# Kernel optimization log

Hardware: AMD Instinct MI355X
Metric: run time of the kernel (lower is better)

Reference implementation:

```python
import jax, jax.numpy as jnp
import numpy as np

GROUP_SIZE = 64  # int4 precision
QMAX = 7.0       # symmetric int4 quant scale divisor


def setup_inputs() -> dict:
    key = jax.random.key(0)
    ks = jax.random.split(key, 8)
    B, S, C_in, C_out, R = 1, 4096, 3072, 3072, 32
    G = C_in // GROUP_SIZE
    x = jax.random.normal(ks[0], (B, S, C_in), dtype=jnp.float32)
    # unpacked int4 weight codes in [0,16); reference subtracts 8 -> signed int4 [-8,7]
    qweight = jax.random.randint(ks[1], (C_out, C_in), 0, 16, dtype=jnp.int32)
    # small positive per-group, per-out-channel weight scales
    wscales = jax.random.uniform(ks[2], (G, C_out), dtype=jnp.float32) * 0.01 + 0.001
    # positive smoothing factors bounded away from zero
    smooth_factor = jax.random.uniform(ks[3], (C_in,), dtype=jnp.float32) + 0.5
    proj_down = jax.random.normal(ks[4], (C_in, R), dtype=jnp.float32) * (1.0 / np.sqrt(C_in))
    proj_up = jax.random.normal(ks[5], (C_out, R), dtype=jnp.float32) * (1.0 / np.sqrt(R))
    bias = jax.random.normal(ks[6], (C_out,), dtype=jnp.float32) * 0.02
    return {
        "x": x,
        "qweight": qweight,
        "wscales": wscales,
        "smooth_factor": smooth_factor,
        "proj_down": proj_down,
        "proj_up": proj_up,
        "bias": bias,
    }


def reference(x, qweight, wscales, smooth_factor, proj_down, proj_up, bias):
    B, S, C = x.shape
    C_out = qweight.shape[0]
    M = B * S
    G = C // GROUP_SIZE

    # --- smoothing: x_hat = x / s (SVDQuant smoothing on activations) ---
    xs = x.reshape(M, C) / smooth_factor  # (M, C)

    # --- low-rank branch hidden state (fused with quantization in CUDA kernel) ---
    lora_act = jnp.einsum('mc,cr->mr', xs, proj_down)  # (M, R)

    # --- dynamic per-token, per-group int4 activation quantization ---
    xg = xs.reshape(M, G, GROUP_SIZE)
    amax = jnp.max(jnp.abs(xg), axis=-1, keepdims=True)          # (M, G, 1)
    ascale = amax / QMAX
    q = jnp.clip(jnp.round(xg / jnp.maximum(ascale, 1e-8)), -8.0, 7.0)
    x_dq = (q * ascale).reshape(M, C)                            # dequantized activations

    # --- weight dequantization: signed int4 codes * per-group/out-channel scales ---
    qw = qweight.astype(jnp.float32) - 8.0                       # (C_out, C) in [-8, 7]
    w_dq = (qw.reshape(C_out, G, GROUP_SIZE) * wscales.T[:, :, None]).reshape(C_out, C)

    # --- quantized GEMM + low-rank correction + bias ---
    out = jnp.einsum('mc,oc->mo', x_dq, w_dq)
    out = out + jnp.einsum('mr,or->mo', lora_act, proj_up) + bias
    return out.reshape(B, S, C_out)
```

## Files before the change

kernel.cpp:

```cpp
#include <hip/hip_runtime.h>
#include <stdint.h>

typedef unsigned short u16;

#define MTOK 4096
#define CIN  3072
#define COUT 3072
#define RANK 32
#define RS   3136
#define LKSPLIT 16
#define LKC (CIN/LKSPLIT)
#define WROWS 6

typedef __attribute__((ext_vector_type(8))) short bf16x8;
typedef __attribute__((ext_vector_type(4))) float f32x4;

__device__ __forceinline__ u16 f2bf(float f) {
  union { float f; unsigned u; } v; v.f = f;
  unsigned r = v.u + 0x7FFFu + ((v.u >> 16) & 1u);
  return (u16)(r >> 16);
}

__device__ __forceinline__ void gload_lds16(const void* g, void* l) {
  __builtin_amdgcn_global_load_lds(
      (const __attribute__((address_space(1))) unsigned int*)g,
      (__attribute__((address_space(3))) unsigned int*)l, 16, 0, 0);
}

__device__ __forceinline__ float quant1(float xs, float ascale, float qd) {
  float q = rintf(xs / qd);
  q = fminf(fmaxf(q, -8.f), 7.f);
  return q * ascale;
}

__global__ __launch_bounds__(256) void prep_kernel(
    const float* __restrict__ x, const float* __restrict__ smooth,
    const int* __restrict__ qw, const float* __restrict__ wsc,
    const float* __restrict__ pd, const float* __restrict__ pu,
    u16* __restrict__ xdq, u16* __restrict__ wdq, u16* __restrict__ pu_bf,
    float* __restrict__ lp)
{
  const int b = blockIdx.x;
  const int t = threadIdx.x;

#pragma unroll
  for (int r = 0; r < WROWS; ++r) {
    const int o = b * WROWS + r;
    const int4* qrow = (const int4*)(qw + (size_t)o * CIN);
    u16* orow = wdq + (size_t)o * RS;
#pragma unroll
    for (int p = 0; p < 3; ++p) {
      const int c4 = p * 256 + t;
      const int g = (c4 * 4) >> 6;
      const float ws = wsc[g * COUT + o];
      const int4 qv = qrow[c4];
      ushort4 ov;
      ov.x = f2bf((float)(qv.x - 8) * ws);
      ov.y = f2bf((float)(qv.y - 8) * ws);
      ov.z = f2bf((float)(qv.z - 8) * ws);
      ov.w = f2bf((float)(qv.w - 8) * ws);
      ((ushort4*)orow)[c4] = ov;
    }
  }
  if (t < WROWS * RANK) {
    const int o = b * WROWS + (t >> 5);
    pu_bf[(size_t)o * RANK + (t & 31)] = f2bf(pu[(size_t)o * RANK + (t & 31)]);
  }

  __shared__ __align__(16) u16 sA[128 * 64];
  __shared__ __align__(16) u16 sB[32 * 64];
  const int m0 = (b >> 4) * 128;
  const int kblk = b & 15;
  const int wave = t >> 6, lane = t & 63;
  const int lm = lane & 15, lkq = (lane >> 4) * 8;

  f32x4 acc[2][2];
  const f32x4 fz = {0.f, 0.f, 0.f, 0.f};
#pragma unroll
  for (int i = 0; i < 2; ++i)
#pragma unroll
    for (int j = 0; j < 2; ++j) acc[i][j] = fz;

  for (int kt = 0; kt < LKC / 64; ++kt) {
    const int k0 = kblk * LKC + kt * 64;
    const int col = (t & 15) * 4;
#pragma unroll
    for (int it = 0; it < 8; ++it) {
      const int row = it * 16 + (t >> 4);
      const float4 xv = *(const float4*)(x + (size_t)(m0 + row) * CIN + k0 + col);
      const float4 sv = *(const float4*)(smooth + k0 + col);
      const float xs0 = xv.x / sv.x, xs1 = xv.y / sv.y;
      const float xs2 = xv.z / sv.z, xs3 = xv.w / sv.w;
      ushort4 ov;
      ov.x = f2bf(xs0); ov.y = f2bf(xs1); ov.z = f2bf(xs2); ov.w = f2bf(xs3);
      *(ushort4*)&sA[row * 64 + col] = ov;
      float a = fmaxf(fmaxf(fabsf(xs0), fabsf(xs1)), fmaxf(fabsf(xs2), fabsf(xs3)));
#pragma unroll
      for (int off = 1; off < 16; off <<= 1) a = fmaxf(a, __shfl_xor(a, off));
      const float ascale = a / 7.0f;
      const float qd = fmaxf(ascale, 1e-8f);
      ushort4 oq;
      oq.x = f2bf(quant1(xs0, ascale, qd));
      oq.y = f2bf(quant1(xs1, ascale, qd));
      oq.z = f2bf(quant1(xs2, ascale, qd));
      oq.w = f2bf(quant1(xs3, ascale, qd));
      *(ushort4*)(xdq + (size_t)(m0 + row) * RS + k0 + col) = oq;
    }
#pragma unroll
    for (int i = 0; i < 8; ++i) {
      const int idx = i * 256 + t;
      const int k = idx >> 5, r = idx & 31;
      sB[r * 64 + k] = f2bf(pd[(size_t)(k0 + k) * RANK + r]);
    }
    __syncthreads();
#pragma unroll
    for (int kk = 0; kk < 2; ++kk) {
      const int ko = kk * 32 + lkq;
      bf16x8 af[2], bfr[2];
#pragma unroll
      for (int i = 0; i < 2; ++i)
        af[i] = *(const bf16x8*)&sA[(wave * 32 + i * 16 + lm) * 64 + ko];
#pragma unroll
      for (int j = 0; j < 2; ++j)
        bfr[j] = *(const bf16x8*)&sB[(j * 16 + lm) * 64 + ko];
#pragma unroll
      for (int i = 0; i < 2; ++i)
#pragma unroll
        for (int j = 0; j < 2; ++j)
          acc[i][j] = __builtin_amdgcn_mfma_f32_16x16x32_bf16(af[i], bfr[j], acc[i][j], 0, 0, 0);
    }
    __syncthreads();
  }
  float* lpk = lp + (size_t)kblk * MTOK * RANK;
#pragma unroll
  for (int i = 0; i < 2; ++i)
#pragma unroll
    for (int j = 0; j < 2; ++j) {
      const int col = j * 16 + lm;
      const int row0 = m0 + wave * 32 + i * 16 + (lane >> 4) * 4;
#pragma unroll
      for (int r = 0; r < 4; ++r)
        lpk[(size_t)(row0 + r) * RANK + col] = acc[i][j][r];
    }
}

__global__ __launch_bounds__(256) void lora_fix_kernel(
    const float* __restrict__ lp, u16* __restrict__ lora_bf)
{
  const int idx = blockIdx.x * 256 + threadIdx.x;
  const int m = idx >> 5, c = idx & 31;
  float s = 0.f;
#pragma unroll
  for (int k = 0; k < LKSPLIT; ++k) s += lp[((size_t)k * MTOK + m) * RANK + c];
  lora_bf[(size_t)m * RANK + c] = f2bf(s);
}


__device__ __forceinline__ void stage_A_half(const u16* __restrict__ g, u16* lds0,
                                             int kt, int half, int buf, int t) {
#pragma unroll
  for (int r = 0; r < 2; ++r) {
    const int id = r * 512 + t;
    const int row = id >> 3;
    const int sl = id & 7;
    const int c16 = sl ^ (row & 7);
    gload_lds16(g + (size_t)(half * 128 + row) * RS + kt * 64 + c16 * 8,
                lds0 + buf * 16384 + half * 8192 + id * 8);
  }
}

__device__ __forceinline__ void stage_B_half(const u16* __restrict__ g, u16* lds0,
                                             int kt, int nh, int buf, int t) {
  u16* base = lds0 + 32768 + buf * 12288 + nh * 6144;
  {
    const int row = t >> 3, sl = t & 7;
    const int c16 = sl ^ (row & 7);
    gload_lds16(g + (size_t)(nh * 96 + row) * RS + kt * 64 + c16 * 8, base + t * 8);
  }
  if (nh ? (t >= 256) : (t < 256)) {
    const int et = t - (nh ? 256 : 0);
    const int row = 64 + (et >> 3), sl = et & 7;
    const int c16 = sl ^ (row & 7);
    gload_lds16(g + (size_t)(nh * 96 + row) * RS + kt * 64 + c16 * 8,
                base + 4096 + et * 8);
  }
}

#define DSA(buf, mh) \
  _Pragma("unroll") for (int i_ = 0; i_ < 2; ++i_) { \
    const int rl = wm * 32 + i_ * 16 + lm; \
    _Pragma("unroll") for (int kk = 0; kk < 2; ++kk) \
      af[i_][kk] = *(const bf16x8*)&lds[(buf)*16384 + (mh)*8192 + rl * 64 + \
                    ((((kk << 2) | q4) ^ (rl & 7)) << 3)]; \
  }

#define DSB(buf, nh, BQ) \
  _Pragma("unroll") for (int j_ = 0; j_ < 3; ++j_) { \
    const int rb = wn * 48 + j_ * 16 + lm; \
    _Pragma("unroll") for (int kk = 0; kk < 2; ++kk) \
      BQ[j_][kk] = *(const bf16x8*)&lds[32768 + (buf)*12288 + (nh)*6144 + rb * 64 + \
                    ((((kk << 2) | q4) ^ (rb & 7)) << 3)]; \
  }

#define MFMA_Q(mh, nh, BQ) \
  __builtin_amdgcn_s_setprio(1); \
  _Pragma("unroll") for (int i_ = 0; i_ < 2; ++i_) \
  _Pragma("unroll") for (int j_ = 0; j_ < 3; ++j_) \
  _Pragma("unroll") for (int kk = 0; kk < 2; ++kk) \
    acc[(mh)*2 + i_][(nh)*3 + j_] = __builtin_amdgcn_mfma_f32_16x16x32_bf16( \
        af[i_][kk], BQ[j_][kk], acc[(mh)*2 + i_][(nh)*3 + j_], 0, 0, 0); \
  __builtin_amdgcn_s_setprio(0);

#define PH_OPEN() \
  __builtin_amdgcn_sched_barrier(0); \
  __builtin_amdgcn_s_barrier(); \
  asm volatile("s_waitcnt lgkmcnt(0)" ::: "memory"); \
  __builtin_amdgcn_sched_barrier(0)

#define PH_CLOSE() \
  __builtin_amdgcn_sched_barrier(0); \
  __builtin_amdgcn_s_barrier(); \
  __builtin_amdgcn_sched_barrier(0)

#define VM7() asm volatile("s_waitcnt vmcnt(7)" ::: "memory")
#define VM0() asm volatile("s_waitcnt vmcnt(0)" ::: "memory")

#define TILE4(cur, S_A0, S_B0, S_B1, S_A1, VMI) do { \
  DSA(cur, 0); DSB(cur, 0, bq0); \
  PH_OPEN(); MFMA_Q(0, 0, bq0); PH_CLOSE(); \
  DSB(cur, 1, bq1); S_A0; S_B0; \
  PH_OPEN(); MFMA_Q(0, 1, bq1); PH_CLOSE(); \
  DSA(cur, 1); S_B1; \
  PH_OPEN(); MFMA_Q(1, 1, bq1); PH_CLOSE(); \
  S_A1; \
  PH_OPEN(); MFMA_Q(1, 0, bq0); VMI; PH_CLOSE(); \
} while (0)

__global__ __launch_bounds__(512, 2) void gemm_kernel(
    const u16* __restrict__ xdq, const u16* __restrict__ wdq,
    const u16* __restrict__ pu_bf, const u16* __restrict__ lora_bf,
    const float* __restrict__ bias, float* __restrict__ out)
{
  __shared__ __align__(16) u16 lds[57344];

  const int t = threadIdx.x;
  const int wid = t >> 6, lane = t & 63;
  const int wm = wid >> 1, wn = wid & 1;
  const int lm = lane & 15, q4 = lane >> 4;

  const int wg = blockIdx.x;
  const int swz = (wg & 7) * 32 + (wg >> 3);
  const int by = swz >> 4, bx = swz & 15;
  const int m0 = by * 256, n0 = bx * 192;

  const u16* Ag = xdq + (size_t)m0 * RS;
  const u16* Bg = wdq + (size_t)n0 * RS;

  f32x4 acc[4][6];
  const f32x4 fz = {0.f, 0.f, 0.f, 0.f};
#pragma unroll
  for (int i = 0; i < 4; ++i)
#pragma unroll
    for (int j = 0; j < 6; ++j) acc[i][j] = fz;

  bf16x8 af[2][2], bq0[3][2], bq1[3][2];

  stage_A_half(Ag, lds, 0, 0, 0, t);
  stage_B_half(Bg, lds, 0, 0, 0, t);
  stage_B_half(Bg, lds, 0, 1, 0, t);
  stage_A_half(Ag, lds, 0, 1, 0, t);
  stage_A_half(Ag, lds, 1, 0, 1, t);
  stage_B_half(Bg, lds, 1, 0, 1, t);
  stage_B_half(Bg, lds, 1, 1, 1, t);
  stage_A_half(Ag, lds, 1, 1, 1, t);
  VM7();
  __builtin_amdgcn_s_barrier();
  __builtin_amdgcn_sched_barrier(0);

  for (int T = 0; T < 46; T += 2) {
    TILE4(0,
          stage_A_half(Ag, lds, T + 2, 0, 0, t),
          stage_B_half(Bg, lds, T + 2, 0, 0, t),
          stage_B_half(Bg, lds, T + 2, 1, 0, t),
          stage_A_half(Ag, lds, T + 2, 1, 0, t),
          VM7());
    TILE4(1,
          stage_A_half(Ag, lds, T + 3, 0, 1, t),
          stage_B_half(Bg, lds, T + 3, 0, 1, t),
          stage_B_half(Bg, lds, T + 3, 1, 1, t),
          stage_A_half(Ag, lds, T + 3, 1, 1, t),
          VM7());
  }
  TILE4(0, (void)0, (void)0, (void)0, (void)0, VM0());
  TILE4(1, (void)0, (void)0, (void)0, (void)0, (void)0);

  bf16x8 bl[6];
#pragma unroll
  for (int b = 0; b < 6; ++b) {
    const int bcol = n0 + (b / 3) * 96 + wn * 48 + (b % 3) * 16 + lm;
    bl[b] = *(const bf16x8*)(pu_bf + (size_t)bcol * RANK + q4 * 8);
  }
#pragma unroll
  for (int a = 0; a < 4; ++a) {
    const int arow = m0 + (a >> 1) * 128 + wm * 32 + (a & 1) * 16 + lm;
    const bf16x8 al = *(const bf16x8*)(lora_bf + (size_t)arow * RANK + q4 * 8);
#pragma unroll
    for (int b = 0; b < 6; ++b)
      acc[a][b] = __builtin_amdgcn_mfma_f32_16x16x32_bf16(al, bl[b], acc[a][b], 0, 0, 0);
  }

#pragma unroll
  for (int b = 0; b < 6; ++b) {
    const int col = n0 + (b / 3) * 96 + wn * 48 + (b % 3) * 16 + lm;
    const float bv = bias[col];
#pragma unroll
    for (int a = 0; a < 4; ++a) {
      const int row0 = m0 + (a >> 1) * 128 + wm * 32 + (a & 1) * 16 + q4 * 4;
#pragma unroll
      for (int r = 0; r < 4; ++r)
        out[(size_t)(row0 + r) * COUT + col] = acc[a][b][r] + bv;
    }
  }
}

extern "C" void kernel_launch(void* const* d_in, const int* in_sizes, int n_in,
                              void* d_out, int out_size, void* d_ws, size_t ws_size,
                              hipStream_t stream) {
  const float* x      = (const float*)d_in[0];
  const int*   qw     = (const int*)d_in[1];
  const float* wsc    = (const float*)d_in[2];
  const float* smooth = (const float*)d_in[3];
  const float* pd     = (const float*)d_in[4];
  const float* pu     = (const float*)d_in[5];
  const float* bias   = (const float*)d_in[6];
  float* out = (float*)d_out;

  u16* xdq     = (u16*)d_ws;
  u16* wdq     = xdq + (size_t)MTOK * RS;
  u16* pu_bf   = wdq + (size_t)COUT * RS;
  u16* lora_bf = pu_bf + (size_t)COUT * RANK;
  float* lp    = (float*)(lora_bf + (size_t)MTOK * RANK);

  prep_kernel<<<512, 256, 0, stream>>>(
      x, smooth, qw, wsc, pd, pu, xdq, wdq, pu_bf, lp);
  lora_fix_kernel<<<MTOK * RANK / 256, 256, 0, stream>>>(lp, lora_bf);
  gemm_kernel<<<256, 512, 0, stream>>>(
      xdq, wdq, pu_bf, lora_bf, bias, out);
}
```

Baseline: 218.3 us.

## Switch GEMM main loop to triple-buffered K=32 tiles with one barrier per tile

The bf16 GEMM main loop moves from double-buffered K=64 tiles, split into four quadrant phases with two barriers each, to triple-buffered K=32 tiles. Each tile now does one stage, one full fragment read and 24 MFMAs, with a single barrier. The LDS swizzle and the vmcnt accounting are reworked to match. The goal is fewer barriers and deeper prefetch to hide global latency, at the cost of less work per barrier and halved K depth per tile, which may leave MFMA bursts too short to cover LDS reads.

```diff
diff --git a/kernel.cpp b/kernel.cpp
--- a/kernel.cpp
+++ b/kernel.cpp
@@ -156,84 +156,70 @@
 }
 
 
-__device__ __forceinline__ void stage_A_half(const u16* __restrict__ g, u16* lds0,
-                                             int kt, int half, int buf, int t) {
+__device__ __forceinline__ void stage32(const u16* __restrict__ Ag,
+                                        const u16* __restrict__ Bg,
+                                        u16* lds, int kt, int buf,
+                                        int t, int wid) {
 #pragma unroll
   for (int r = 0; r < 2; ++r) {
     const int id = r * 512 + t;
-    const int row = id >> 3;
-    const int sl = id & 7;
-    const int c16 = sl ^ (row & 7);
-    gload_lds16(g + (size_t)(half * 128 + row) * RS + kt * 64 + c16 * 8,
-                lds0 + buf * 16384 + half * 8192 + id * 8);
-  }
-}
-
-__device__ __forceinline__ void stage_B_half(const u16* __restrict__ g, u16* lds0,
-                                             int kt, int nh, int buf, int t) {
-  u16* base = lds0 + 32768 + buf * 12288 + nh * 6144;
+    const int row = id >> 2, sl = id & 3;
+    const int c16 = sl ^ ((row >> 1) & 3);
+    gload_lds16(Ag + (size_t)row * RS + kt * 32 + c16 * 8,
+                lds + buf * 8192 + id * 8);
+  }
   {
-    const int row = t >> 3, sl = t & 7;
-    const int c16 = sl ^ (row & 7);
-    gload_lds16(g + (size_t)(nh * 96 + row) * RS + kt * 64 + c16 * 8, base + t * 8);
-  }
-  if (nh ? (t >= 256) : (t < 256)) {
-    const int et = t - (nh ? 256 : 0);
-    const int row = 64 + (et >> 3), sl = et & 7;
-    const int c16 = sl ^ (row & 7);
-    gload_lds16(g + (size_t)(nh * 96 + row) * RS + kt * 64 + c16 * 8,
-                base + 4096 + et * 8);
-  }
-}
-
-#define DSA(buf, mh) \
-  _Pragma("unroll") for (int i_ = 0; i_ < 2; ++i_) { \
-    const int rl = wm * 32 + i_ * 16 + lm; \
-    _Pragma("unroll") for (int kk = 0; kk < 2; ++kk) \
-      af[i_][kk] = *(const bf16x8*)&lds[(buf)*16384 + (mh)*8192 + rl * 64 + \
-                    ((((kk << 2) | q4) ^ (rl & 7)) << 3)]; \
-  }
-
-#define DSB(buf, nh, BQ) \
-  _Pragma("unroll") for (int j_ = 0; j_ < 3; ++j_) { \
-    const int rb = wn * 48 + j_ * 16 + lm; \
-    _Pragma("unroll") for (int kk = 0; kk < 2; ++kk) \
-      BQ[j_][kk] = *(const bf16x8*)&lds[32768 + (buf)*12288 + (nh)*6144 + rb * 64 + \
-                    ((((kk << 2) | q4) ^ (rb & 7)) << 3)]; \
-  }
-
-#define MFMA_Q(mh, nh, BQ) \
+    const int row = t >> 2, sl = t & 3;
+    const int c16 = sl ^ ((row >> 1) & 3);
+    gload_lds16(Bg + (size_t)row * RS + kt * 32 + c16 * 8,
+                lds + 24576 + buf * 6144 + t * 8);
+  }
+  if (wid >= 4) {
+    const int c = 256 + t;
+    const int row = c >> 2, sl = c & 3;
+    const int c16 = sl ^ ((row >> 1) & 3);
+    gload_lds16(Bg + (size_t)row * RS + kt * 32 + c16 * 8,
+                lds + 24576 + buf * 6144 + c * 8);
+  }
+}
+
+#define RD_ALL(BUF) \
+  _Pragma("unroll") for (int a_ = 0; a_ < 4; ++a_) { \
+    const int rl = (a_ >> 1) * 128 + wm * 32 + (a_ & 1) * 16 + lm; \
+    aF[a_] = *(const bf16x8*)&lds[(BUF) * 8192 + rl * 32 + \
+                                  ((q4 ^ ((rl >> 1) & 3)) << 3)]; \
+  } \
+  _Pragma("unroll") for (int b_ = 0; b_ < 6; ++b_) { \
+    const int rb = (b_ / 3) * 96 + wn * 48 + (b_ % 3) * 16 + lm; \
+    bF[b_] = *(const bf16x8*)&lds[24576 + (BUF) * 6144 + rb * 32 + \
+                                  ((q4 ^ ((rb >> 1) & 3)) << 3)]; \
+  }
+
+#define MFMA_ALL() \
   __builtin_amdgcn_s_setprio(1); \
-  _Pragma("unroll") for (int i_ = 0; i_ < 2; ++i_) \
-  _Pragma("unroll") for (int j_ = 0; j_ < 3; ++j_) \
-  _Pragma("unroll") for (int kk = 0; kk < 2; ++kk) \
-    acc[(mh)*2 + i_][(nh)*3 + j_] = __builtin_amdgcn_mfma_f32_16x16x32_bf16( \
-        af[i_][kk], BQ[j_][kk], acc[(mh)*2 + i_][(nh)*3 + j_], 0, 0, 0); \
+  _Pragma("unroll") for (int a_ = 0; a_ < 4; ++a_) \
+  _Pragma("unroll") for (int b_ = 0; b_ < 6; ++b_) \
+    acc[a_][b_] = __builtin_amdgcn_mfma_f32_16x16x32_bf16( \
+        aF[a_], bF[b_], acc[a_][b_], 0, 0, 0); \
   __builtin_amdgcn_s_setprio(0);
 
-#define PH_OPEN() \
-  __builtin_amdgcn_sched_barrier(0); \
-  __builtin_amdgcn_s_barrier(); \
-  asm volatile("s_waitcnt lgkmcnt(0)" ::: "memory"); \
-  __builtin_amdgcn_sched_barrier(0)
-
-#define PH_CLOSE() \
-  __builtin_amdgcn_sched_barrier(0); \
-  __builtin_amdgcn_s_barrier(); \
-  __builtin_amdgcn_sched_barrier(0)
-
-#define VM7() asm volatile("s_waitcnt vmcnt(7)" ::: "memory")
+#define VMB() do { \
+  if (wid < 4) asm volatile("s_waitcnt vmcnt(3)" ::: "memory"); \
+  else         asm volatile("s_waitcnt vmcnt(4)" ::: "memory"); \
+} while (0)
 #define VM0() asm volatile("s_waitcnt vmcnt(0)" ::: "memory")
-
-#define TILE4(cur, S_A0, S_B0, S_B1, S_A1, VMI) do { \
-  DSA(cur, 0); DSB(cur, 0, bq0); \
-  PH_OPEN(); MFMA_Q(0, 0, bq0); PH_CLOSE(); \
-  DSB(cur, 1, bq1); S_A0; S_B0; \
-  PH_OPEN(); MFMA_Q(0, 1, bq1); PH_CLOSE(); \
-  DSA(cur, 1); S_B1; \
-  PH_OPEN(); MFMA_Q(1, 1, bq1); PH_CLOSE(); \
-  S_A1; \
-  PH_OPEN(); MFMA_Q(1, 0, bq0); VMI; PH_CLOSE(); \
+#define LK0() asm volatile("s_waitcnt lgkmcnt(0)" ::: "memory")
+
+#define TILE3(CB, SB, KT2, DOSTAGE, VMW, DOBAR) do { \
+  if (DOSTAGE) stage32(Ag, Bg, lds, (KT2), (SB), t, wid); \
+  RD_ALL(CB); \
+  MFMA_ALL(); \
+  LK0(); \
+  VMW; \
+  if (DOBAR) { \
+    __builtin_amdgcn_s_barrier(); \
+    __builtin_amdgcn_sched_barrier(0); \
+  } \
 } while (0)
 
 __global__ __launch_bounds__(512, 2) void gemm_kernel(
@@ -241,7 +227,7 @@
     const u16* __restrict__ pu_bf, const u16* __restrict__ lora_bf,
     const float* __restrict__ bias, float* __restrict__ out)
 {
-  __shared__ __align__(16) u16 lds[57344];
+  __shared__ __align__(16) u16 lds[43008];
 
   const int t = threadIdx.x;
   const int wid = t >> 6, lane = t & 63;
@@ -263,62 +249,51 @@
 #pragma unroll
     for (int j = 0; j < 6; ++j) acc[i][j] = fz;
 
-  bf16x8 af[2][2], bq0[3][2], bq1[3][2];
-
-  stage_A_half(Ag, lds, 0, 0, 0, t);
-  stage_B_half(Bg, lds, 0, 0, 0, t);
-  stage_B_half(Bg, lds, 0, 1, 0, t);
-  stage_A_half(Ag, lds, 0, 1, 0, t);
-  stage_A_half(Ag, lds, 1, 0, 1, t);
-  stage_B_half(Bg, lds, 1, 0, 1, t);
-  stage_B_half(Bg, lds, 1, 1, 1, t);
-  stage_A_half(Ag, lds, 1, 1, 1, t);
-  VM7();
+  bf16x8 aF[4], bF[6];
+
+  stage32(Ag, Bg, lds, 0, 0, t, wid);
+  stage32(Ag, Bg, lds, 1, 1, t, wid);
+  VMB();
   __builtin_amdgcn_s_barrier();
   __builtin_amdgcn_sched_barrier(0);
 
-  for (int T = 0; T < 46; T += 2) {
-    TILE4(0,
-          stage_A_half(Ag, lds, T + 2, 0, 0, t),
-          stage_B_half(Bg, lds, T + 2, 0, 0, t),
-          stage_B_half(Bg, lds, T + 2, 1, 0, t),
-          stage_A_half(Ag, lds, T + 2, 1, 0, t),
-          VM7());
-    TILE4(1,
-          stage_A_half(Ag, lds, T + 3, 0, 1, t),
-          stage_B_half(Bg, lds, T + 3, 0, 1, t),
-          stage_B_half(Bg, lds, T + 3, 1, 1, t),
-          stage_A_half(Ag, lds, T + 3, 1, 1, t),
-          VM7());
-  }
-  TILE4(0, (void)0, (void)0, (void)0, (void)0, VM0());
-  TILE4(1, (void)0, (void)0, (void)0, (void)0, (void)0);
+  for (int T = 0; T < 90; T += 3) {
+    TILE3(0, 2, T + 2, 1, VMB(), 1);
+    TILE3(1, 0, T + 3, 1, VMB(), 1);
+    TILE3(2, 1, T + 4, 1, VMB(), 1);
+  }
+  TILE3(0, 2, 92, 1, VMB(), 1);
+  TILE3(1, 0, 93, 1, VMB(), 1);
+  TILE3(2, 1, 94, 1, VMB(), 1);
+  TILE3(0, 2, 95, 1, VMB(), 1);
+  TILE3(1, 2, 0,  0, VM0(), 1);
+  TILE3(2, 2, 0,  0, (void)0, 0);
 
   bf16x8 bl[6];
 #pragma unroll
-  for (int b = 0; b < 6; ++b) {
-    const int bcol = n0 + (b / 3) * 96 + wn * 48 + (b % 3) * 16 + lm;
-    bl[b] = *(const bf16x8*)(pu_bf + (size_t)bcol * RANK + q4 * 8);
+  for (int bb = 0; bb < 6; ++bb) {
+    const int bcol = n0 + (bb / 3) * 96 + wn * 48 + (bb % 3) * 16 + lm;
+    bl[bb] = *(const bf16x8*)(pu_bf + (size_t)bcol * RANK + q4 * 8);
   }
 #pragma unroll
   for (int a = 0; a < 4; ++a) {
     const int arow = m0 + (a >> 1) * 128 + wm * 32 + (a & 1) * 16 + lm;
     const bf16x8 al = *(const bf16x8*)(lora_bf + (size_t)arow * RANK + q4 * 8);
 #pragma unroll
-    for (int b = 0; b < 6; ++b)
-      acc[a][b] = __builtin_amdgcn_mfma_f32_16x16x32_bf16(al, bl[b], acc[a][b], 0, 0, 0);
-  }
-
-#pragma unroll
-  for (int b = 0; b < 6; ++b) {
-    const int col = n0 + (b / 3) * 96 + wn * 48 + (b % 3) * 16 + lm;
+    for (int bb = 0; bb < 6; ++bb)
+      acc[a][bb] = __builtin_amdgcn_mfma_f32_16x16x32_bf16(al, bl[bb], acc[a][bb], 0, 0, 0);
+  }
+
+#pragma unroll
+  for (int bb = 0; bb < 6; ++bb) {
+    const int col = n0 + (bb / 3) * 96 + wn * 48 + (bb % 3) * 16 + lm;
     const float bv = bias[col];
 #pragma unroll
     for (int a = 0; a < 4; ++a) {
       const int row0 = m0 + (a >> 1) * 128 + wm * 32 + (a & 1) * 16 + q4 * 4;
 #pragma unroll
       for (int r = 0; r < 4; ++r)
-        out[(size_t)(row0 + r) * COUT + col] = acc[a][b][r] + bv;
+        out[(size_t)(row0 + r) * COUT + col] = acc[a][bb][r] + bv;
     }
   }
 }
```

Result: no change. 220.4 us (+0.9%).
